# Optimization experiments

Measured on AMD Instinct MI355X. Metric: run time of the kernel, lower is better.

Reference implementation:

```python
import jax, jax.numpy as jnp
import numpy as np
import math

D_MODEL = 256
NHEAD = 8
HEAD = D_MODEL // NHEAD


def make_pe(H, W):
    # temp_bug_fix=False quirk: (-log(1e4)/d_model) // 2 == -1.0 (floor div applied after the divide)
    fac = (-math.log(10000.0) / D_MODEL) // 2
    div = jnp.exp(jnp.arange(0, D_MODEL // 2, 2, dtype=jnp.float32) * fac)[:, None, None]  # [64,1,1]
    xp = jnp.broadcast_to(jnp.arange(1, W + 1, dtype=jnp.float32)[None, :], (H, W))[None]  # [1,H,W]
    yp = jnp.broadcast_to(jnp.arange(1, H + 1, dtype=jnp.float32)[:, None], (H, W))[None]
    pe = jnp.zeros((D_MODEL, H, W), dtype=jnp.float32)
    pe = pe.at[0::4].set(jnp.sin(xp * div))
    pe = pe.at[1::4].set(jnp.cos(xp * div))
    pe = pe.at[2::4].set(jnp.sin(yp * div))
    pe = pe.at[3::4].set(jnp.cos(yp * div))
    return pe[None]  # [1,C,H,W]


def layer_norm(x, g, b, eps=1e-5):
    mu = x.mean(-1, keepdims=True)
    var = ((x - mu) ** 2).mean(-1, keepdims=True)
    return (x - mu) * jax.lax.rsqrt(var + eps) * g + b


def linear_attention(q, k, v, eps=1e-6):
    # q: [N,L,H,D], k/v: [N,S,H,D]
    Q = jax.nn.elu(q) + 1.0
    K = jax.nn.elu(k) + 1.0
    S = v.shape[1]
    v = v / S
    KV = jnp.einsum('nshd,nshv->nhdv', K, v)                      # [N,H,D,D]
    Z = 1.0 / (jnp.einsum('nlhd,nhd->nlh', Q, K.sum(axis=1)) + eps)
    return jnp.einsum('nlhd,nhdv,nlh->nlhv', Q, KV, Z) * S        # [N,L,H,D]


def encoder_layer(x, src, Wq, Wk, Wv, Wm, W1, W2, g1, b1, g2, b2):
    N, L, _ = x.shape
    q = (x @ Wq).reshape(N, L, NHEAD, HEAD)
    k = (src @ Wk).reshape(N, -1, NHEAD, HEAD)
    v = (src @ Wv).reshape(N, -1, NHEAD, HEAD)
    msg = linear_attention(q, k, v).reshape(N, L, D_MODEL) @ Wm
    msg = layer_norm(msg, g1, b1)
    msg = jax.nn.relu(jnp.concatenate([x, msg], axis=-1) @ W1) @ W2
    msg = layer_norm(msg, g2, b2)
    return x + msg


def setup_inputs() -> dict:
    key = jax.random.key(0)
    ks = jax.random.split(key, 10)
    N, H, W = 16, 80, 60
    sc = 1.0 / math.sqrt(D_MODEL)
    return {
        'feat0': jax.random.normal(ks[0], (N, D_MODEL, H, W), dtype=jnp.float32),
        'feat1': jax.random.normal(ks[1], (N, D_MODEL, H, W), dtype=jnp.float32),
        'Wq': jax.random.normal(ks[2], (2, D_MODEL, D_MODEL), dtype=jnp.float32) * sc,
        'Wk': jax.random.normal(ks[3], (2, D_MODEL, D_MODEL), dtype=jnp.float32) * sc,
        'Wv': jax.random.normal(ks[4], (2, D_MODEL, D_MODEL), dtype=jnp.float32) * sc,
        'Wm': jax.random.normal(ks[5], (2, D_MODEL, D_MODEL), dtype=jnp.float32) * sc,
        'W1': jax.random.normal(ks[6], (2, 2 * D_MODEL, D_MODEL), dtype=jnp.float32) * sc,
        'W2': jax.random.normal(ks[7], (2, D_MODEL, D_MODEL), dtype=jnp.float32) * sc,
        'g1': jnp.ones((2, D_MODEL), dtype=jnp.float32),
        'b1': jnp.zeros((2, D_MODEL), dtype=jnp.float32),
        'g2': jnp.ones((2, D_MODEL), dtype=jnp.float32),
        'b2': jnp.zeros((2, D_MODEL), dtype=jnp.float32),
    }


def reference(feat0, feat1, Wq, Wk, Wv, Wm, W1, W2, g1, b1, g2, b2):
    N, C, H, W = feat0.shape
    pe = make_pe(H, W)
    f0 = (feat0 + pe).transpose(0, 2, 3, 1).reshape(N, H * W, C)
    f1 = (feat1 + pe).transpose(0, 2, 3, 1).reshape(N, -1, C)
    for i in range(2):
        f0 = encoder_layer(f0, f1, Wq[i], Wk[i], Wv[i], Wm[i], W1[i], W2[i], g1[i], b1[i], g2[i], b2[i])
    return f0.reshape(N, H, W, C).transpose(0, 3, 1, 2)
```

## Files before the change

### kernel.cpp

```cpp
#include <hip/hip_runtime.h>
#include <math.h>

#define NB 16
#define HH 80
#define WW 60
#define HWSZ (HH * WW)
#define CC 256
#define MTOT (NB * HWSZ)
#define KVF (16 * 8 * 32 * 32)
#define KSF (16 * 8 * 32)
#define BUF ((size_t)MTOT * CC)

typedef unsigned short u16;
typedef __attribute__((ext_vector_type(8))) short short8;
typedef __attribute__((ext_vector_type(4))) float floatx4;

__device__ __forceinline__ float bf2f(u16 u) {
    union { unsigned int i; float f; } v; v.i = ((unsigned int)u) << 16; return v.f;
}
__device__ __forceinline__ u16 f2bf(float f) {
    union { unsigned int i; float f; } v; v.f = f;
    unsigned int u = v.i;
    u += 0x7FFFu + ((u >> 16) & 1u);
    return (u16)(u >> 16);
}
__device__ __forceinline__ float elu1(float x) { return x > 0.f ? x + 1.f : expf(x); }

__device__ __forceinline__ float pe_val(int c, int l) {
    const int h = l / WW, w = l - h * WW;
    const int j = c >> 2, sel = c & 3;
    const float dv = expf(-2.0f * (float)j);
    const float pos = (sel < 2) ? (float)(w + 1) : (float)(h + 1);
    const float arg = pos * dv;
    return (sel & 1) ? cosf(arg) : sinf(arg);
}

__global__ __launch_bounds__(256) void add_pe_transpose(const float* __restrict__ in,
                                                        float* __restrict__ outf,
                                                        u16* __restrict__ outb)
{
    __shared__ float tile[32][33];
    const int n = blockIdx.z;
    const int c0 = blockIdx.y * 32;
    const int l0 = blockIdx.x * 32;
    const int tx = threadIdx.x, ty = threadIdx.y;
#pragma unroll
    for (int i = 0; i < 4; ++i) {
        const int cl = ty + i * 8;
        tile[cl][tx] = in[(size_t)n * CC * HWSZ + (size_t)(c0 + cl) * HWSZ + l0 + tx];
    }
    __syncthreads();
#pragma unroll
    for (int i = 0; i < 4; ++i) {
        const int ll = ty + i * 8;
        const int l = l0 + ll;
        const int c = c0 + tx;
        const float val = tile[tx][ll] + pe_val(c, l);
        const size_t idx = ((size_t)n * HWSZ + l) * CC + c;
        if (outf) outf[idx] = val;
        outb[idx] = f2bf(val);
    }
}

__global__ __launch_bounds__(256) void out_transpose(const float* __restrict__ in,
                                                     float* __restrict__ out)
{
    __shared__ float tile[32][33];
    const int n = blockIdx.z;
    const int c0 = blockIdx.y * 32;
    const int l0 = blockIdx.x * 32;
    const int tx = threadIdx.x, ty = threadIdx.y;
#pragma unroll
    for (int i = 0; i < 4; ++i) {
        const int ll = ty + i * 8;
        tile[ll][tx] = in[((size_t)n * HWSZ + l0 + ll) * CC + c0 + tx];
    }
    __syncthreads();
#pragma unroll
    for (int i = 0; i < 4; ++i) {
        const int cl = ty + i * 8;
        out[(size_t)n * CC * HWSZ + (size_t)(c0 + cl) * HWSZ + l0 + tx] = tile[tx][cl];
    }
}

__global__ __launch_bounds__(256) void convert_wt(const float* __restrict__ W,
                                                  u16* __restrict__ WT, int K)
{
    __shared__ float tile[32][33];
    const int k0 = blockIdx.x * 32;
    const int n0 = blockIdx.y * 32;
    const int tx = threadIdx.x, ty = threadIdx.y;
#pragma unroll
    for (int i = 0; i < 4; ++i)
        tile[ty + i * 8][tx] = W[(size_t)(k0 + ty + i * 8) * 256 + n0 + tx];
    __syncthreads();
#pragma unroll
    for (int i = 0; i < 4; ++i)
        WT[(size_t)(n0 + ty + i * 8) * K + k0 + tx] = f2bf(tile[tx][ty + i * 8]);
}

__global__ __launch_bounds__(256) void zero_kernel(float* __restrict__ p, int n)
{
    const int i = blockIdx.x * 256 + threadIdx.x;
    if (i < n) p[i] = 0.f;
}

__global__ __launch_bounds__(256) void gemm_mfma(const u16* __restrict__ A0,
                                                 const u16* __restrict__ A1,
                                                 const u16* __restrict__ WT,
                                                 u16* __restrict__ C,
                                                 int K, int relu)
{
    __shared__ u16 As[128 * 32];
    __shared__ u16 Bs[128 * 32];
    const int t = threadIdx.x;
    const int row0 = blockIdx.y * 128;
    const int col0 = blockIdx.x * 128;
    const int w = t >> 6, lane = t & 63;
    const int wr = (w >> 1) * 64, wc = (w & 1) * 64;
    const int quad = lane >> 4, lrow = lane & 15;
    const int sm = t >> 2, skc = (t & 3) * 8;

    const floatx4 zero = {0.f, 0.f, 0.f, 0.f};
    floatx4 acc[4][4];
#pragma unroll
    for (int i = 0; i < 4; ++i)
#pragma unroll
        for (int j = 0; j < 4; ++j) acc[i][j] = zero;

    const size_t arow0 = (size_t)(row0 + sm) * 256 + skc;
    const size_t arow1 = (size_t)(row0 + 64 + sm) * 256 + skc;
    const size_t brow0 = (size_t)(col0 + sm) * K + skc;
    const size_t brow1 = (size_t)(col0 + 64 + sm) * K + skc;

    uint4 ra0 = *(const uint4*)(A0 + arow0);
    uint4 ra1 = *(const uint4*)(A0 + arow1);
    uint4 rb0 = *(const uint4*)(WT + brow0);
    uint4 rb1 = *(const uint4*)(WT + brow1);

    for (int k0 = 0; k0 < K; k0 += 32) {
        __syncthreads();
        *(uint4*)&As[sm * 32 + skc] = ra0;
        *(uint4*)&As[(64 + sm) * 32 + skc] = ra1;
        *(uint4*)&Bs[sm * 32 + skc] = rb0;
        *(uint4*)&Bs[(64 + sm) * 32 + skc] = rb1;
        __syncthreads();
        const int kn = k0 + 32;
        if (kn < K) {
            const u16* Abn = (A1 != nullptr && kn >= 256) ? (A1 + (kn - 256)) : (A0 + kn);
            ra0 = *(const uint4*)(Abn + arow0);
            ra1 = *(const uint4*)(Abn + arow1);
            rb0 = *(const uint4*)(WT + brow0 + kn);
            rb1 = *(const uint4*)(WT + brow1 + kn);
        }
        short8 af[4], bfv[4];
#pragma unroll
        for (int i = 0; i < 4; ++i) {
            af[i]  = *(const short8*)&As[(wr + i * 16 + lrow) * 32 + quad * 8];
            bfv[i] = *(const short8*)&Bs[(wc + i * 16 + lrow) * 32 + quad * 8];
        }
#pragma unroll
        for (int i = 0; i < 4; ++i)
#pragma unroll
            for (int j = 0; j < 4; ++j)
                acc[i][j] = __builtin_amdgcn_mfma_f32_16x16x32_bf16(af[i], bfv[j], acc[i][j], 0, 0, 0);
    }

#pragma unroll
    for (int i = 0; i < 4; ++i) {
        const int rbase = row0 + wr + i * 16 + quad * 4;
#pragma unroll
        for (int j = 0; j < 4; ++j) {
            const int cc = col0 + wc + j * 16 + lrow;
#pragma unroll
            for (int r = 0; r < 4; ++r) {
                float x = acc[i][j][r];
                if (relu) x = fmaxf(x, 0.f);
                C[(size_t)(rbase + r) * 256 + cc] = f2bf(x);
            }
        }
    }
}

#define SCHUNK 480
__global__ __launch_bounds__(256) void kv_kernel(const u16* __restrict__ kbuf,
                                                 const u16* __restrict__ vbuf,
                                                 float* __restrict__ KV,
                                                 float* __restrict__ Ksum)
{
    __shared__ float Kls[16][32];
    __shared__ float Vls[16][32];
    const int n = blockIdx.z, h = blockIdx.y;
    const int s0 = blockIdx.x * SCHUNK;
    const int t = threadIdx.x;
    const int lr = t >> 5;
    const int lc = t & 31;
    const int d = t >> 3;
    const int e0 = (t & 7) * 4;
    const float invS = 1.0f / 4800.0f;
    float acc0 = 0.f, acc1 = 0.f, acc2 = 0.f, acc3 = 0.f, ks = 0.f;
    for (int it = 0; it < SCHUNK / 16; ++it) {
        const int sb = s0 + it * 16;
#pragma unroll
        for (int rr = 0; rr < 2; ++rr) {
            const int s = sb + lr + rr * 8;
            const size_t base = ((size_t)(n * HWSZ + s)) * 256 + h * 32 + lc;
            Kls[lr + rr * 8][lc] = elu1(bf2f(kbuf[base]));
            Vls[lr + rr * 8][lc] = bf2f(vbuf[base]) * invS;
        }
        __syncthreads();
#pragma unroll
        for (int ss = 0; ss < 16; ++ss) {
            const float kval = Kls[ss][d];
            acc0 += kval * Vls[ss][e0 + 0];
            acc1 += kval * Vls[ss][e0 + 1];
            acc2 += kval * Vls[ss][e0 + 2];
            acc3 += kval * Vls[ss][e0 + 3];
            if (e0 == 0) ks += kval;
        }
        __syncthreads();
    }
    float* kvp = KV + ((size_t)(n * 8 + h) * 32 + d) * 32 + e0;
    atomicAdd(kvp + 0, acc0);
    atomicAdd(kvp + 1, acc1);
    atomicAdd(kvp + 2, acc2);
    atomicAdd(kvp + 3, acc3);
    if (e0 == 0) atomicAdd(&Ksum[(size_t)(n * 8 + h) * 32 + d], ks);
}

__global__ __launch_bounds__(256) void kv_finalize(const float* __restrict__ KV,
                                                   u16* __restrict__ KVThi,
                                                   u16* __restrict__ KVTlo)
{
    const int nh = blockIdx.x;
    const int t = threadIdx.x;
    const int d = t >> 3, e0 = (t & 7) * 4;
    const float4 v = *(const float4*)&KV[(size_t)nh * 1024 + d * 32 + e0];
    const float vv[4] = {v.x, v.y, v.z, v.w};
#pragma unroll
    for (int j = 0; j < 4; ++j) {
        const int e = e0 + j;
        const float x = vv[j];
        const u16 hi = f2bf(x);
        const float lo = x - bf2f(hi);
        KVThi[(size_t)nh * 1024 + e * 32 + d] = hi;
        KVTlo[(size_t)nh * 1024 + e * 32 + d] = f2bf(lo);
    }
}

__global__ __launch_bounds__(256) void attn_apply(u16* __restrict__ q,
                                                  const u16* __restrict__ KVThi,
                                                  const u16* __restrict__ KVTlo,
                                                  const float* __restrict__ Ksum)
{
    const int t = threadIdx.x;
    const int row0b = blockIdx.x * 64;
    const int n = row0b / HWSZ;
    const int w = t >> 6, lane = t & 63;
    const int quad = lane >> 4, lrow = lane & 15;
    const int row0 = row0b + w * 16;

    __shared__ float Ks[256];
    Ks[t] = Ksum[(size_t)n * 256 + t];
    __syncthreads();

    const floatx4 zero = {0.f, 0.f, 0.f, 0.f};
#pragma unroll
    for (int h = 0; h < 8; ++h) {
        const size_t qoff = (size_t)(row0 + lrow) * 256 + h * 32 + quad * 8;
        const ushort4 u0 = *(const ushort4*)&q[qoff];
        const ushort4 u1 = *(const ushort4*)&q[qoff + 4];
        float qf[8];
        qf[0] = elu1(bf2f(u0.x)); qf[1] = elu1(bf2f(u0.y));
        qf[2] = elu1(bf2f(u0.z)); qf[3] = elu1(bf2f(u0.w));
        qf[4] = elu1(bf2f(u1.x)); qf[5] = elu1(bf2f(u1.y));
        qf[6] = elu1(bf2f(u1.z)); qf[7] = elu1(bf2f(u1.w));
        short8 a;
#pragma unroll
        for (int j = 0; j < 8; ++j) a[j] = (short)f2bf(qf[j]);

        float zp = 0.f;
#pragma unroll
        for (int j = 0; j < 8; ++j) zp += qf[j] * Ks[h * 32 + quad * 8 + j];
        zp += __shfl_xor(zp, 16, 64);
        zp += __shfl_xor(zp, 32, 64);

        const size_t kvb = (size_t)(n * 8 + h) * 32;
        const short8 bh0 = *(const short8*)&KVThi[(kvb + lrow) * 32 + quad * 8];
        const short8 bh1 = *(const short8*)&KVThi[(kvb + 16 + lrow) * 32 + quad * 8];
        const short8 bl0 = *(const short8*)&KVTlo[(kvb + lrow) * 32 + quad * 8];
        const short8 bl1 = *(const short8*)&KVTlo[(kvb + 16 + lrow) * 32 + quad * 8];

        floatx4 acc0 = __builtin_amdgcn_mfma_f32_16x16x32_bf16(a, bh0, zero, 0, 0, 0);
        acc0 = __builtin_amdgcn_mfma_f32_16x16x32_bf16(a, bl0, acc0, 0, 0, 0);
        floatx4 acc1 = __builtin_amdgcn_mfma_f32_16x16x32_bf16(a, bh1, zero, 0, 0, 0);
        acc1 = __builtin_amdgcn_mfma_f32_16x16x32_bf16(a, bl1, acc1, 0, 0, 0);

#pragma unroll
        for (int r = 0; r < 4; ++r) {
            const float zden = __shfl(zp, quad * 4 + r, 64);
            const float sc = 4800.0f / (zden + 1e-6f);
            const size_t ob = (size_t)(row0 + quad * 4 + r) * 256 + h * 32;
            q[ob + lrow]      = f2bf(acc0[r] * sc);
            q[ob + 16 + lrow] = f2bf(acc1[r] * sc);
        }
    }
}

__device__ __forceinline__ float wave_sum(float v)
{
#pragma unroll
    for (int off = 32; off > 0; off >>= 1) v += __shfl_xor(v, off, 64);
    return v;
}

__global__ __launch_bounds__(256) void ln_inplace(u16* __restrict__ x,
                                                  const float* __restrict__ g,
                                                  const float* __restrict__ b)
{
    const int t = threadIdx.x;
    const int wv = t >> 6, lane = t & 63;
    const int row0 = blockIdx.x * 32 + wv * 8;
    const int c0 = lane * 4;
    const float4 gv = *(const float4*)&g[c0];
    const float4 bv = *(const float4*)&b[c0];
#pragma unroll
    for (int r = 0; r < 8; ++r) {
        const size_t base = (size_t)(row0 + r) * 256 + c0;
        const ushort4 u = *(const ushort4*)&x[base];
        const float v0 = bf2f(u.x), v1 = bf2f(u.y), v2 = bf2f(u.z), v3 = bf2f(u.w);
        const float mu = wave_sum(v0 + v1 + v2 + v3) * (1.0f / 256.0f);
        const float d0 = v0 - mu, d1 = v1 - mu, d2 = v2 - mu, d3 = v3 - mu;
        const float var = wave_sum(d0 * d0 + d1 * d1 + d2 * d2 + d3 * d3) * (1.0f / 256.0f);
        const float rst = rsqrtf(var + 1e-5f);
        ushort4 o;
        o.x = f2bf(d0 * rst * gv.x + bv.x);
        o.y = f2bf(d1 * rst * gv.y + bv.y);
        o.z = f2bf(d2 * rst * gv.z + bv.z);
        o.w = f2bf(d3 * rst * gv.w + bv.w);
        *(ushort4*)&x[base] = o;
    }
}

__global__ __launch_bounds__(256) void ln_resid(const u16* __restrict__ x,
                                                const float* __restrict__ g,
                                                const float* __restrict__ b,
                                                float* __restrict__ f0,
                                                u16* __restrict__ f0b)
{
    const int t = threadIdx.x;
    const int wv = t >> 6, lane = t & 63;
    const int row0 = blockIdx.x * 32 + wv * 8;
    const int c0 = lane * 4;
    const float4 gv = *(const float4*)&g[c0];
    const float4 bv = *(const float4*)&b[c0];
#pragma unroll
    for (int r = 0; r < 8; ++r) {
        const size_t base = (size_t)(row0 + r) * 256 + c0;
        const ushort4 u = *(const ushort4*)&x[base];
        const float v0 = bf2f(u.x), v1 = bf2f(u.y), v2 = bf2f(u.z), v3 = bf2f(u.w);
        const float mu = wave_sum(v0 + v1 + v2 + v3) * (1.0f / 256.0f);
        const float d0 = v0 - mu, d1 = v1 - mu, d2 = v2 - mu, d3 = v3 - mu;
        const float var = wave_sum(d0 * d0 + d1 * d1 + d2 * d2 + d3 * d3) * (1.0f / 256.0f);
        const float rst = rsqrtf(var + 1e-5f);
        float4 f = *(const float4*)&f0[base];
        f.x += d0 * rst * gv.x + bv.x;
        f.y += d1 * rst * gv.y + bv.y;
        f.z += d2 * rst * gv.z + bv.z;
        f.w += d3 * rst * gv.w + bv.w;
        *(float4*)&f0[base] = f;
        ushort4 o;
        o.x = f2bf(f.x); o.y = f2bf(f.y); o.z = f2bf(f.z); o.w = f2bf(f.w);
        *(ushort4*)&f0b[base] = o;
    }
}

extern "C" void kernel_launch(void* const* d_in, const int* in_sizes, int n_in,
                              void* d_out, int out_size, void* d_ws, size_t ws_size,
                              hipStream_t stream)
{
    const float* feat0 = (const float*)d_in[0];
    const float* feat1 = (const float*)d_in[1];
    const float* Wq = (const float*)d_in[2];
    const float* Wk = (const float*)d_in[3];
    const float* Wv = (const float*)d_in[4];
    const float* Wm = (const float*)d_in[5];
    const float* W1 = (const float*)d_in[6];
    const float* W2 = (const float*)d_in[7];
    const float* g1 = (const float*)d_in[8];
    const float* b1 = (const float*)d_in[9];
    const float* g2 = (const float*)d_in[10];
    const float* b2 = (const float*)d_in[11];

    float* ws = (float*)d_ws;
    float* KV = ws;
    float* Ksum = KV + KVF;
    u16* Wb = (u16*)(Ksum + KSF);
    const size_t WBE = 458752;
    float* f0 = ws + (KVF + KSF) + WBE;
    u16* f0b = (u16*)(f0 + BUF);
    u16* f1b = f0b + BUF;
    u16* KVThi = f1b + BUF;
    u16* KVTlo = KVThi + KVF;
    u16* kb16 = (u16*)d_out;
    u16* vb16 = kb16 + BUF;

    const dim3 tb(32, 8);
    const dim3 tgrid(HWSZ / 32, CC / 32, NB);
    add_pe_transpose<<<tgrid, tb, 0, stream>>>(feat0, f0, f0b);
    add_pe_transpose<<<tgrid, tb, 0, stream>>>(feat1, nullptr, f1b);

    for (int i = 0; i < 2; ++i) {
        u16* WqT = Wb + (size_t)i * WBE;
        u16* WkT = WqT + 65536;
        u16* WvT = WkT + 65536;
        u16* WmT = WvT + 65536;
        u16* W1T = WmT + 65536;
        u16* W2T = W1T + 131072;
        convert_wt<<<dim3(8, 8),  tb, 0, stream>>>(Wq + (size_t)i * 65536,  WqT, 256);
        convert_wt<<<dim3(8, 8),  tb, 0, stream>>>(Wk + (size_t)i * 65536,  WkT, 256);
        convert_wt<<<dim3(8, 8),  tb, 0, stream>>>(Wv + (size_t)i * 65536,  WvT, 256);
        convert_wt<<<dim3(8, 8),  tb, 0, stream>>>(Wm + (size_t)i * 65536,  WmT, 256);
        convert_wt<<<dim3(16, 8), tb, 0, stream>>>(W1 + (size_t)i * 131072, W1T, 512);
        convert_wt<<<dim3(8, 8),  tb, 0, stream>>>(W2 + (size_t)i * 65536,  W2T, 256);
    }

    const dim3 ggrid(2, MTOT / 128);
    for (int i = 0; i < 2; ++i) {
        u16* WqT = Wb + (size_t)i * WBE;
        u16* WkT = WqT + 65536;
        u16* WvT = WkT + 65536;
        u16* WmT = WvT + 65536;
        u16* W1T = WmT + 65536;
        u16* W2T = W1T + 131072;

        gemm_mfma<<<ggrid, 256, 0, stream>>>(f1b, nullptr, WkT, kb16, 256, 0);
        gemm_mfma<<<ggrid, 256, 0, stream>>>(f1b, nullptr, WvT, vb16, 256, 0);

        zero_kernel<<<(KVF + KSF + 255) / 256, 256, 0, stream>>>(KV, KVF + KSF);
        kv_kernel<<<dim3(HWSZ / SCHUNK, 8, NB), 256, 0, stream>>>(kb16, vb16, KV, Ksum);
        kv_finalize<<<128, 256, 0, stream>>>(KV, KVThi, KVTlo);

        gemm_mfma<<<ggrid, 256, 0, stream>>>(f0b, nullptr, WqT, kb16, 256, 0);
        attn_apply<<<MTOT / 64, 256, 0, stream>>>(kb16, KVThi, KVTlo, Ksum);

        gemm_mfma<<<ggrid, 256, 0, stream>>>(kb16, nullptr, WmT, vb16, 256, 0);
        ln_inplace<<<MTOT / 32, 256, 0, stream>>>(vb16, g1 + i * 256, b1 + i * 256);

        gemm_mfma<<<ggrid, 256, 0, stream>>>(f0b, vb16, W1T, kb16, 512, 1);
        gemm_mfma<<<ggrid, 256, 0, stream>>>(kb16, nullptr, W2T, vb16, 256, 0);
        ln_resid<<<MTOT / 32, 256, 0, stream>>>(vb16, g2 + i * 256, b2 + i * 256, f0, f0b);
    }

    out_transpose<<<tgrid, tb, 0, stream>>>(f0, (float*)d_out);
}
```

Measured before the change: 844.3 us.

## Register-tile KV accumulation with 4x4 outer products and prefetched vector loads

Rewrites the KV reduction kernel so each thread accumulates a 4x4 block of K^T V from float4 LDS reads, with the four waves each handling a separate slice of the 32 staged rows. Global loads are vectorized to ushort4 and the next chunk is prefetched into registers during compute. Per-wave partials are combined through shared memory before the atomics, which cuts LDS traffic per FMA. This adds a final LDS reduction and more shared memory per block.

```diff
diff --git a/kernel.cpp b/kernel.cpp
--- a/kernel.cpp
+++ b/kernel.cpp
@@ -188,44 +188,84 @@
                                                  float* __restrict__ KV,
                                                  float* __restrict__ Ksum)
 {
-    __shared__ float Kls[16][32];
-    __shared__ float Vls[16][32];
+    __shared__ float Kls[32][32];
+    __shared__ float Vls[32][32];
+    __shared__ float red[4][1024];
+    __shared__ float ksred[4][32];
     const int n = blockIdx.z, h = blockIdx.y;
     const int s0 = blockIdx.x * SCHUNK;
     const int t = threadIdx.x;
-    const int lr = t >> 5;
-    const int lc = t & 31;
-    const int d = t >> 3;
-    const int e0 = (t & 7) * 4;
+    const int wv = t >> 6, lane = t & 63;
+    const int dg = lane >> 3, eg = lane & 7;
+    const int d0 = dg * 4, e0 = eg * 4;
+    const int sl = t >> 3;
+    const int c0 = (t & 7) * 4;
     const float invS = 1.0f / 4800.0f;
-    float acc0 = 0.f, acc1 = 0.f, acc2 = 0.f, acc3 = 0.f, ks = 0.f;
-    for (int it = 0; it < SCHUNK / 16; ++it) {
-        const int sb = s0 + it * 16;
-#pragma unroll
-        for (int rr = 0; rr < 2; ++rr) {
-            const int s = sb + lr + rr * 8;
-            const size_t base = ((size_t)(n * HWSZ + s)) * 256 + h * 32 + lc;
-            Kls[lr + rr * 8][lc] = elu1(bf2f(kbuf[base]));
-            Vls[lr + rr * 8][lc] = bf2f(vbuf[base]) * invS;
-        }
+
+    float acc[4][4] = {{0.f}};
+    float ks[4] = {0.f, 0.f, 0.f, 0.f};
+
+    const size_t sbase = ((size_t)(n * HWSZ + s0 + sl)) * 256 + h * 32 + c0;
+    ushort4 kr = *(const ushort4*)&kbuf[sbase];
+    ushort4 vr = *(const ushort4*)&vbuf[sbase];
+
+    for (int it = 0; it < SCHUNK / 32; ++it) {
+        float4 kf, vf;
+        kf.x = elu1(bf2f(kr.x)); kf.y = elu1(bf2f(kr.y));
+        kf.z = elu1(bf2f(kr.z)); kf.w = elu1(bf2f(kr.w));
+        vf.x = bf2f(vr.x) * invS; vf.y = bf2f(vr.y) * invS;
+        vf.z = bf2f(vr.z) * invS; vf.w = bf2f(vr.w) * invS;
+        *(float4*)&Kls[sl][c0] = kf;
+        *(float4*)&Vls[sl][c0] = vf;
         __syncthreads();
-#pragma unroll
-        for (int ss = 0; ss < 16; ++ss) {
-            const float kval = Kls[ss][d];
-            acc0 += kval * Vls[ss][e0 + 0];
-            acc1 += kval * Vls[ss][e0 + 1];
-            acc2 += kval * Vls[ss][e0 + 2];
-            acc3 += kval * Vls[ss][e0 + 3];
-            if (e0 == 0) ks += kval;
+        if (it + 1 < SCHUNK / 32) {
+            const size_t nb = sbase + (size_t)(it + 1) * 32 * 256;
+            kr = *(const ushort4*)&kbuf[nb];
+            vr = *(const ushort4*)&vbuf[nb];
+        }
+#pragma unroll
+        for (int i = 0; i < 8; ++i) {
+            const int ss = wv * 8 + i;
+            const float4 kq = *(const float4*)&Kls[ss][d0];
+            const float4 vq = *(const float4*)&Vls[ss][e0];
+            acc[0][0] += kq.x * vq.x; acc[0][1] += kq.x * vq.y;
+            acc[0][2] += kq.x * vq.z; acc[0][3] += kq.x * vq.w;
+            acc[1][0] += kq.y * vq.x; acc[1][1] += kq.y * vq.y;
+            acc[1][2] += kq.y * vq.z; acc[1][3] += kq.y * vq.w;
+            acc[2][0] += kq.z * vq.x; acc[2][1] += kq.z * vq.y;
+            acc[2][2] += kq.z * vq.z; acc[2][3] += kq.z * vq.w;
+            acc[3][0] += kq.w * vq.x; acc[3][1] += kq.w * vq.y;
+            acc[3][2] += kq.w * vq.z; acc[3][3] += kq.w * vq.w;
+            ks[0] += kq.x; ks[1] += kq.y; ks[2] += kq.z; ks[3] += kq.w;
         }
         __syncthreads();
     }
-    float* kvp = KV + ((size_t)(n * 8 + h) * 32 + d) * 32 + e0;
-    atomicAdd(kvp + 0, acc0);
-    atomicAdd(kvp + 1, acc1);
-    atomicAdd(kvp + 2, acc2);
-    atomicAdd(kvp + 3, acc3);
-    if (e0 == 0) atomicAdd(&Ksum[(size_t)(n * 8 + h) * 32 + d], ks);
+
+#pragma unroll
+    for (int i = 0; i < 4; ++i) {
+        float4 rv;
+        rv.x = acc[i][0]; rv.y = acc[i][1]; rv.z = acc[i][2]; rv.w = acc[i][3];
+        *(float4*)&red[wv][(d0 + i) * 32 + e0] = rv;
+    }
+    if (eg == 0) {
+#pragma unroll
+        for (int i = 0; i < 4; ++i) ksred[wv][d0 + i] = ks[i];
+    }
+    __syncthreads();
+
+    const float4 r0 = *(const float4*)&red[0][t * 4];
+    const float4 r1 = *(const float4*)&red[1][t * 4];
+    const float4 r2 = *(const float4*)&red[2][t * 4];
+    const float4 r3 = *(const float4*)&red[3][t * 4];
+    float* kvp = KV + (size_t)(n * 8 + h) * 1024 + t * 4;
+    atomicAdd(kvp + 0, r0.x + r1.x + r2.x + r3.x);
+    atomicAdd(kvp + 1, r0.y + r1.y + r2.y + r3.y);
+    atomicAdd(kvp + 2, r0.z + r1.z + r2.z + r3.z);
+    atomicAdd(kvp + 3, r0.w + r1.w + r2.w + r3.w);
+    if (t < 32) {
+        const float s = ksred[0][t] + ksred[1][t] + ksred[2][t] + ksred[3][t];
+        atomicAdd(&Ksum[(size_t)(n * 8 + h) * 32 + t], s);
+    }
 }
 
 __global__ __launch_bounds__(256) void kv_finalize(const float* __restrict__ KV,
```

Result: no change. 843.1 us (-0.1%).

## Restructure KV reduction with register tiling and deterministic partial sums

Applied to the files above, without the earlier changes.

Rewrites the K^T V reduction so each block covers all 8 heads over a 240-row chunk. Rows are loaded with vectorized 16-byte loads and the next tile is prefetched into registers, and each thread accumulates a 4x8 register tile instead of 4 scalars. Float atomics and the zero-fill kernel are replaced by per-chunk partial buffers that the finalize kernel sums. This cuts LDS traffic per FMA, global load instructions and atomic contention, at the cost of extra workspace and more reads in finalize.

```diff
diff --git a/kernel.cpp b/kernel.cpp
--- a/kernel.cpp
+++ b/kernel.cpp
@@ -11,6 +11,10 @@
 #define KSF (16 * 8 * 32)
 #define BUF ((size_t)MTOT * CC)
 
+#define KVCH 20
+#define KVSCH 240
+#define KVTILES 15
+
 typedef unsigned short u16;
 typedef __attribute__((ext_vector_type(8))) short short8;
 typedef __attribute__((ext_vector_type(4))) float floatx4;
@@ -97,12 +101,6 @@
 #pragma unroll
     for (int i = 0; i < 4; ++i)
         WT[(size_t)(n0 + ty + i * 8) * K + k0 + tx] = f2bf(tile[tx][ty + i * 8]);
-}
-
-__global__ __launch_bounds__(256) void zero_kernel(float* __restrict__ p, int n)
-{
-    const int i = blockIdx.x * 256 + threadIdx.x;
-    if (i < n) p[i] = 0.f;
 }
 
 __global__ __launch_bounds__(256) void gemm_mfma(const u16* __restrict__ A0,
@@ -182,61 +180,116 @@
     }
 }
 
-#define SCHUNK 480
 __global__ __launch_bounds__(256) void kv_kernel(const u16* __restrict__ kbuf,
                                                  const u16* __restrict__ vbuf,
-                                                 float* __restrict__ KV,
-                                                 float* __restrict__ Ksum)
-{
-    __shared__ float Kls[16][32];
-    __shared__ float Vls[16][32];
-    const int n = blockIdx.z, h = blockIdx.y;
-    const int s0 = blockIdx.x * SCHUNK;
+                                                 float* __restrict__ Part,
+                                                 float* __restrict__ PartKs)
+{
+    __shared__ float Kls[16][256];
+    __shared__ float Vls[16][256];
+    const int chunk = blockIdx.x, n = blockIdx.y;
     const int t = threadIdx.x;
-    const int lr = t >> 5;
-    const int lc = t & 31;
-    const int d = t >> 3;
-    const int e0 = (t & 7) * 4;
+    const int sr = t >> 5;
+    const int sc = (t & 31) * 8;
+    const int h = t >> 5;
+    const int wl = t & 31;
+    const int d0 = (wl >> 2) * 4;
+    const int e0 = (wl & 3) * 8;
     const float invS = 1.0f / 4800.0f;
-    float acc0 = 0.f, acc1 = 0.f, acc2 = 0.f, acc3 = 0.f, ks = 0.f;
-    for (int it = 0; it < SCHUNK / 16; ++it) {
-        const int sb = s0 + it * 16;
-#pragma unroll
-        for (int rr = 0; rr < 2; ++rr) {
-            const int s = sb + lr + rr * 8;
-            const size_t base = ((size_t)(n * HWSZ + s)) * 256 + h * 32 + lc;
-            Kls[lr + rr * 8][lc] = elu1(bf2f(kbuf[base]));
-            Vls[lr + rr * 8][lc] = bf2f(vbuf[base]) * invS;
+
+    float acc[4][8];
+#pragma unroll
+    for (int i = 0; i < 4; ++i)
+#pragma unroll
+        for (int j = 0; j < 8; ++j) acc[i][j] = 0.f;
+    float ks0 = 0.f, ks1 = 0.f, ks2 = 0.f, ks3 = 0.f;
+
+    const size_t gbase = ((size_t)n * HWSZ + (size_t)chunk * KVSCH) * 256;
+    const size_t off0 = (size_t)sr * 256 + sc;
+    const size_t off1 = off0 + 8 * 256;
+
+    uint4 k0 = *(const uint4*)(kbuf + gbase + off0);
+    uint4 k1 = *(const uint4*)(kbuf + gbase + off1);
+    uint4 v0 = *(const uint4*)(vbuf + gbase + off0);
+    uint4 v1 = *(const uint4*)(vbuf + gbase + off1);
+
+    for (int tile = 0; tile < KVTILES; ++tile) {
+        {
+            const u16* p = (const u16*)&k0;
+            float4 a, b;
+            a.x = elu1(bf2f(p[0])); a.y = elu1(bf2f(p[1])); a.z = elu1(bf2f(p[2])); a.w = elu1(bf2f(p[3]));
+            b.x = elu1(bf2f(p[4])); b.y = elu1(bf2f(p[5])); b.z = elu1(bf2f(p[6])); b.w = elu1(bf2f(p[7]));
+            *(float4*)&Kls[sr][sc] = a; *(float4*)&Kls[sr][sc + 4] = b;
+            p = (const u16*)&k1;
+            a.x = elu1(bf2f(p[0])); a.y = elu1(bf2f(p[1])); a.z = elu1(bf2f(p[2])); a.w = elu1(bf2f(p[3]));
+            b.x = elu1(bf2f(p[4])); b.y = elu1(bf2f(p[5])); b.z = elu1(bf2f(p[6])); b.w = elu1(bf2f(p[7]));
+            *(float4*)&Kls[sr + 8][sc] = a; *(float4*)&Kls[sr + 8][sc + 4] = b;
+            p = (const u16*)&v0;
+            a.x = bf2f(p[0]) * invS; a.y = bf2f(p[1]) * invS; a.z = bf2f(p[2]) * invS; a.w = bf2f(p[3]) * invS;
+            b.x = bf2f(p[4]) * invS; b.y = bf2f(p[5]) * invS; b.z = bf2f(p[6]) * invS; b.w = bf2f(p[7]) * invS;
+            *(float4*)&Vls[sr][sc] = a; *(float4*)&Vls[sr][sc + 4] = b;
+            p = (const u16*)&v1;
+            a.x = bf2f(p[0]) * invS; a.y = bf2f(p[1]) * invS; a.z = bf2f(p[2]) * invS; a.w = bf2f(p[3]) * invS;
+            b.x = bf2f(p[4]) * invS; b.y = bf2f(p[5]) * invS; b.z = bf2f(p[6]) * invS; b.w = bf2f(p[7]) * invS;
+            *(float4*)&Vls[sr + 8][sc] = a; *(float4*)&Vls[sr + 8][sc + 4] = b;
         }
         __syncthreads();
-#pragma unroll
-        for (int ss = 0; ss < 16; ++ss) {
-            const float kval = Kls[ss][d];
-            acc0 += kval * Vls[ss][e0 + 0];
-            acc1 += kval * Vls[ss][e0 + 1];
-            acc2 += kval * Vls[ss][e0 + 2];
-            acc3 += kval * Vls[ss][e0 + 3];
-            if (e0 == 0) ks += kval;
+        if (tile + 1 < KVTILES) {
+            const size_t nb = gbase + (size_t)(tile + 1) * 16 * 256;
+            k0 = *(const uint4*)(kbuf + nb + off0);
+            k1 = *(const uint4*)(kbuf + nb + off1);
+            v0 = *(const uint4*)(vbuf + nb + off0);
+            v1 = *(const uint4*)(vbuf + nb + off1);
+        }
+#pragma unroll
+        for (int s = 0; s < 16; ++s) {
+            const float4 kq  = *(const float4*)&Kls[s][h * 32 + d0];
+            const float4 vq0 = *(const float4*)&Vls[s][h * 32 + e0];
+            const float4 vq1 = *(const float4*)&Vls[s][h * 32 + e0 + 4];
+            acc[0][0] += kq.x * vq0.x; acc[0][1] += kq.x * vq0.y; acc[0][2] += kq.x * vq0.z; acc[0][3] += kq.x * vq0.w;
+            acc[0][4] += kq.x * vq1.x; acc[0][5] += kq.x * vq1.y; acc[0][6] += kq.x * vq1.z; acc[0][7] += kq.x * vq1.w;
+            acc[1][0] += kq.y * vq0.x; acc[1][1] += kq.y * vq0.y; acc[1][2] += kq.y * vq0.z; acc[1][3] += kq.y * vq0.w;
+            acc[1][4] += kq.y * vq1.x; acc[1][5] += kq.y * vq1.y; acc[1][6] += kq.y * vq1.z; acc[1][7] += kq.y * vq1.w;
+            acc[2][0] += kq.z * vq0.x; acc[2][1] += kq.z * vq0.y; acc[2][2] += kq.z * vq0.z; acc[2][3] += kq.z * vq0.w;
+            acc[2][4] += kq.z * vq1.x; acc[2][5] += kq.z * vq1.y; acc[2][6] += kq.z * vq1.z; acc[2][7] += kq.z * vq1.w;
+            acc[3][0] += kq.w * vq0.x; acc[3][1] += kq.w * vq0.y; acc[3][2] += kq.w * vq0.z; acc[3][3] += kq.w * vq0.w;
+            acc[3][4] += kq.w * vq1.x; acc[3][5] += kq.w * vq1.y; acc[3][6] += kq.w * vq1.z; acc[3][7] += kq.w * vq1.w;
+            ks0 += kq.x; ks1 += kq.y; ks2 += kq.z; ks3 += kq.w;
         }
         __syncthreads();
     }
-    float* kvp = KV + ((size_t)(n * 8 + h) * 32 + d) * 32 + e0;
-    atomicAdd(kvp + 0, acc0);
-    atomicAdd(kvp + 1, acc1);
-    atomicAdd(kvp + 2, acc2);
-    atomicAdd(kvp + 3, acc3);
-    if (e0 == 0) atomicAdd(&Ksum[(size_t)(n * 8 + h) * 32 + d], ks);
-}
-
-__global__ __launch_bounds__(256) void kv_finalize(const float* __restrict__ KV,
+
+    const size_t pbase = ((size_t)(n * KVCH + chunk) * 8 + h) * 1024;
+#pragma unroll
+    for (int i = 0; i < 4; ++i) {
+        float4 w0, w1;
+        w0.x = acc[i][0]; w0.y = acc[i][1]; w0.z = acc[i][2]; w0.w = acc[i][3];
+        w1.x = acc[i][4]; w1.y = acc[i][5]; w1.z = acc[i][6]; w1.w = acc[i][7];
+        *(float4*)&Part[pbase + (d0 + i) * 32 + e0]     = w0;
+        *(float4*)&Part[pbase + (d0 + i) * 32 + e0 + 4] = w1;
+    }
+    if (e0 == 0) {
+        float* pk = PartKs + (size_t)(n * KVCH + chunk) * 256 + h * 32 + d0;
+        pk[0] = ks0; pk[1] = ks1; pk[2] = ks2; pk[3] = ks3;
+    }
+}
+
+__global__ __launch_bounds__(256) void kv_finalize(const float* __restrict__ Part,
+                                                   const float* __restrict__ PartKs,
                                                    u16* __restrict__ KVThi,
-                                                   u16* __restrict__ KVTlo)
+                                                   u16* __restrict__ KVTlo,
+                                                   float* __restrict__ Ksum)
 {
     const int nh = blockIdx.x;
+    const int n = nh >> 3, h = nh & 7;
     const int t = threadIdx.x;
     const int d = t >> 3, e0 = (t & 7) * 4;
-    const float4 v = *(const float4*)&KV[(size_t)nh * 1024 + d * 32 + e0];
-    const float vv[4] = {v.x, v.y, v.z, v.w};
+    float4 s = {0.f, 0.f, 0.f, 0.f};
+    for (int c = 0; c < KVCH; ++c) {
+        const float4 p = *(const float4*)&Part[(((size_t)(n * KVCH + c)) * 8 + h) * 1024 + d * 32 + e0];
+        s.x += p.x; s.y += p.y; s.z += p.z; s.w += p.w;
+    }
+    const float vv[4] = {s.x, s.y, s.z, s.w};
 #pragma unroll
     for (int j = 0; j < 4; ++j) {
         const int e = e0 + j;
@@ -245,6 +298,12 @@
         const float lo = x - bf2f(hi);
         KVThi[(size_t)nh * 1024 + e * 32 + d] = hi;
         KVTlo[(size_t)nh * 1024 + e * 32 + d] = f2bf(lo);
+    }
+    if ((t & 7) == 0) {
+        float ksv = 0.f;
+        for (int c = 0; c < KVCH; ++c)
+            ksv += PartKs[((size_t)(n * KVCH + c)) * 256 + h * 32 + d];
+        Ksum[(size_t)n * 256 + h * 32 + d] = ksv;
     }
 }
 
@@ -393,11 +452,12 @@
     const float* b2 = (const float*)d_in[11];
 
     float* ws = (float*)d_ws;
-    float* KV = ws;
-    float* Ksum = KV + KVF;
-    u16* Wb = (u16*)(Ksum + KSF);
+    float* Ksum = ws;
+    float* Part = ws + KSF;
+    float* PartKs = Part + (size_t)NB * KVCH * 8192;
+    u16* Wb = (u16*)(PartKs + (size_t)NB * KVCH * 256);
     const size_t WBE = 458752;
-    float* f0 = ws + (KVF + KSF) + WBE;
+    float* f0 = (float*)(Wb + 2 * WBE);
     u16* f0b = (u16*)(f0 + BUF);
     u16* f1b = f0b + BUF;
     u16* KVThi = f1b + BUF;
@@ -437,9 +497,8 @@
         gemm_mfma<<<ggrid, 256, 0, stream>>>(f1b, nullptr, WkT, kb16, 256, 0);
         gemm_mfma<<<ggrid, 256, 0, stream>>>(f1b, nullptr, WvT, vb16, 256, 0);
 
-        zero_kernel<<<(KVF + KSF + 255) / 256, 256, 0, stream>>>(KV, KVF + KSF);
-        kv_kernel<<<dim3(HWSZ / SCHUNK, 8, NB), 256, 0, stream>>>(kb16, vb16, KV, Ksum);
-        kv_finalize<<<128, 256, 0, stream>>>(KV, KVThi, KVTlo);
+        kv_kernel<<<dim3(KVCH, NB), 256, 0, stream>>>(kb16, vb16, Part, PartKs);
+        kv_finalize<<<128, 256, 0, stream>>>(Part, PartKs, KVThi, KVTlo, Ksum);
 
         gemm_mfma<<<ggrid, 256, 0, stream>>>(f0b, nullptr, WqT, kb16, 256, 0);
         attn_apply<<<MTOT / 64, 256, 0, stream>>>(kb16, KVThi, KVTlo, Ksum);
```

Measured after the change: 837.7 us. About the same (-0.8%).
